# Kernel tuning notes

Measured on AMD Instinct MI355X. Metric: run time of the kernel, lower is better.

The kernel has to match this reference:

```python
import jax, jax.numpy as jnp
import numpy as np

ALPHA = 1.5
TEMPERATURE = 1.0
N_ITER = 25
N_EMBED = 2048
NUM_EXPERTS = 64
N_TOKENS = 32768


def entmax_bisect(X, alpha=ALPHA, n_iter=N_ITER):
    """Faithful port of entmax.entmax_bisect forward (dim=-1)."""
    d = X.shape[-1]
    inv = 1.0 / (alpha - 1.0)
    Xa = X * (alpha - 1.0)
    max_val = jnp.max(Xa, axis=-1, keepdims=True)
    # _gp(1, alpha) = 1 ; _gp(1/d, alpha) = (1/d)**(1/(alpha-1))
    tau_lo = max_val - 1.0
    tau_hi = max_val - (1.0 / d) ** inv

    def p(tau):
        return jnp.clip(Xa - tau, 0.0, None) ** inv

    f_lo = jnp.sum(p(tau_lo), axis=-1, keepdims=True) - 1.0
    dm0 = tau_hi - tau_lo

    def body(carry, _):
        tau_lo, dm = carry
        dm = dm * 0.5
        tau_m = tau_lo + dm
        p_m = p(tau_m)
        f_m = jnp.sum(p_m, axis=-1, keepdims=True) - 1.0
        mask = (f_m * f_lo) >= 0
        tau_lo = jnp.where(mask, tau_m, tau_lo)
        return (tau_lo, dm), tau_m

    (tau_lo, dm), tau_ms = jax.lax.scan(body, (tau_lo, dm0), None, length=n_iter)
    tau_m_last = tau_ms[-1]  # [..., 1] tau used for the returned p_m in torch loop
    p_m = p(tau_m_last)
    # ensure_sum_one
    p_m = p_m / jnp.sum(p_m, axis=-1, keepdims=True)
    return p_m


def setup_inputs() -> dict:
    key = jax.random.key(0)
    kx, kw, kb = jax.random.split(key, 3)
    x = jax.random.normal(kx, (N_TOKENS, N_EMBED), dtype=jnp.float32)
    # nn.Linear default init: U(-1/sqrt(fan_in), 1/sqrt(fan_in))
    bound = 1.0 / np.sqrt(N_EMBED)
    W = jax.random.uniform(kw, (NUM_EXPERTS, N_EMBED), dtype=jnp.float32, minval=-bound, maxval=bound)
    b = jax.random.uniform(kb, (NUM_EXPERTS,), dtype=jnp.float32, minval=-bound, maxval=bound)
    return {"x": x, "W": W, "b": b}


def reference(x, W, b):
    logits = jnp.einsum("td,ed->te", x, W) + b  # [T, E]
    scaled_logits = logits / TEMPERATURE
    return entmax_bisect(scaled_logits)
```

## Files before the change

kernel.cpp:

```cpp
#include <hip/hip_runtime.h>
#include <hip/hip_bf16.h>
#include <stdint.h>

typedef _Float16 half8 __attribute__((ext_vector_type(8)));
typedef float    f32x4 __attribute__((ext_vector_type(4)));

#define N_EMBED   2048
#define N_EXP     64
#define KCHUNK    64
#define NKC       (N_EMBED / KCHUNK)
#define GCH       16
#define TILEB     8192
#define LGT_STRIDE 68
#define LGT_FLOATS (64 * LGT_STRIDE)

__global__ __launch_bounds__(256) void convert_w_kernel(
        const float* __restrict__ W, uint8_t* __restrict__ wsimg) {
    int tid = blockIdx.x * 256 + threadIdx.x;
    int e   = tid >> 8;
    int d0  = (tid & 255) * 8;
    int kc  = d0 >> 6;
    int dd0 = d0 & 63;
    const float* src = W + e * N_EMBED + d0;
    float4 f0 = *(const float4*)(src);
    float4 f1 = *(const float4*)(src + 4);
    float v[8] = {f0.x, f0.y, f0.z, f0.w, f1.x, f1.y, f1.z, f1.w};
    union { _Float16 h[8]; uint4 u; } hv;
#pragma unroll
    for (int j = 0; j < 8; ++j) hv.h[j] = (_Float16)(0.5f * v[j]);
    uint32_t off = (uint32_t)((e * 128 + dd0 * 2) ^ ((e & 7) << 4));
    *(uint4*)(wsimg + (size_t)kc * TILEB + off) = hv.u;
}

__device__ __forceinline__ half8 cvt8(const float4& p, const float4& q) {
    half8 h;
    h[0] = (_Float16)p.x; h[1] = (_Float16)p.y;
    h[2] = (_Float16)p.z; h[3] = (_Float16)p.w;
    h[4] = (_Float16)q.x; h[5] = (_Float16)q.y;
    h[6] = (_Float16)q.z; h[7] = (_Float16)q.w;
    return h;
}

__global__ __launch_bounds__(512, 4) void router_kernel(
        const float* __restrict__ x, const uint8_t* __restrict__ img,
        const float* __restrict__ bias, float* __restrict__ out) {
    __shared__ uint8_t lds[2 * LGT_FLOATS * 4];

    const int tid  = threadIdx.x;
    const int wave = tid >> 6;
    const int lane = tid & 63;
    const int l15  = lane & 15;
    const int l4   = lane >> 4;
    const int g    = wave >> 2;
    const int q    = wave & 3;
    const int rowbase = blockIdx.x * 64;
    const float* xrow = x + (size_t)(rowbase + q * 16 + l15) * N_EMBED
                          + g * (GCH * KCHUNK) + l4 * 8;
    uint8_t* lbase = lds + g * 2 * TILEB;

    uint32_t boff[4][2];
#pragma unroll
    for (int t = 0; t < 4; ++t)
#pragma unroll
        for (int s = 0; s < 2; ++s)
            boff[t][s] = (uint32_t)(((16 * t + l15) * 128 + s * 64 + l4 * 16)
                                    ^ ((l15 & 7) << 4));

    f32x4 acc[4];
#pragma unroll
    for (int t = 0; t < 4; ++t) acc[t] = (f32x4){0.f, 0.f, 0.f, 0.f};

    const int tg  = tid >> 8;
    const int t8  = tid & 255;
    auto STAGE = [&](int i, int buf) {
        const uint8_t* gsrc = img + (size_t)(tg * GCH + i) * TILEB;
        uint8_t* dst = lds + tg * 2 * TILEB + buf * TILEB;
#pragma unroll
        for (int j = 0; j < 2; ++j) {
            __builtin_amdgcn_global_load_lds(
                (const __attribute__((address_space(1))) void*)(gsrc + j * 4096 + t8 * 16),
                (__attribute__((address_space(3))) void*)(dst + j * 4096 + t8 * 16),
                16, 0, 0);
        }
    };
    auto LOADA = [&](int i, float4& a0, float4& a1, float4& a2, float4& a3) {
        const float* ap = xrow + i * KCHUNK;
        a0 = *(const float4*)(ap);
        a1 = *(const float4*)(ap + 4);
        a2 = *(const float4*)(ap + 32);
        a3 = *(const float4*)(ap + 36);
    };
    auto MFMAS = [&](int buf, const half8& a0, const half8& a1) {
        const uint8_t* lb = lbase + (size_t)buf * TILEB;
#pragma unroll
        for (int s = 0; s < 2; ++s) {
            half8 ah = s ? a1 : a0;
#pragma unroll
            for (int t = 0; t < 4; ++t) {
                half8 bh = *(const half8*)(lb + boff[t][s]);
                acc[t] = __builtin_amdgcn_mfma_f32_16x16x32_f16(ah, bh, acc[t], 0, 0, 0);
            }
        }
    };

    float4 A0, A1, A2, A3, B0, B1, B2, B3;

    STAGE(0, 0);
    __builtin_amdgcn_sched_barrier(0);
    LOADA(0, A0, A1, A2, A3);
    LOADA(1, B0, B1, B2, B3);
    __builtin_amdgcn_sched_barrier(0);
    asm volatile("s_waitcnt vmcnt(8)" ::: "memory");
    __builtin_amdgcn_s_barrier();
    __builtin_amdgcn_sched_barrier(0);

#pragma unroll 1
    for (int i = 0; i < GCH - 2; i += 2) {
        STAGE(i + 1, (i + 1) & 1);
        __builtin_amdgcn_sched_barrier(0);
        {
            half8 a0 = cvt8(A0, A1);
            half8 a1 = cvt8(A2, A3);
            LOADA(i + 2, A0, A1, A2, A3);
            MFMAS(i & 1, a0, a1);
        }
        asm volatile("s_waitcnt vmcnt(4) lgkmcnt(0)" ::: "memory");
        __builtin_amdgcn_s_barrier();
        __builtin_amdgcn_sched_barrier(0);

        STAGE(i + 2, i & 1);
        __builtin_amdgcn_sched_barrier(0);
        {
            half8 a0 = cvt8(B0, B1);
            half8 a1 = cvt8(B2, B3);
            LOADA(i + 3, B0, B1, B2, B3);
            MFMAS((i + 1) & 1, a0, a1);
        }
        asm volatile("s_waitcnt vmcnt(4) lgkmcnt(0)" ::: "memory");
        __builtin_amdgcn_s_barrier();
        __builtin_amdgcn_sched_barrier(0);
    }

    STAGE(GCH - 1, 1);
    __builtin_amdgcn_sched_barrier(0);
    {
        half8 a0 = cvt8(A0, A1);
        half8 a1 = cvt8(A2, A3);
        MFMAS(0, a0, a1);
    }
    asm volatile("s_waitcnt vmcnt(0) lgkmcnt(0)" ::: "memory");
    __builtin_amdgcn_s_barrier();
    __builtin_amdgcn_sched_barrier(0);
    {
        half8 a0 = cvt8(B0, B1);
        half8 a1 = cvt8(B2, B3);
        MFMAS(1, a0, a1);
    }

    __syncthreads();
    {
        float* lgt = (float*)lds + g * LGT_FLOATS;
#pragma unroll
        for (int t = 0; t < 4; ++t)
#pragma unroll
            for (int r = 0; r < 4; ++r)
                lgt[(q * 16 + l4 * 4 + r) * LGT_STRIDE + t * 16 + l15] = acc[t][r];
    }
    __syncthreads();

    const float* L0 = (const float*)lds;
    const float* L1 = L0 + LGT_FLOATS;
    const int row_local = wave * 8 + (lane >> 3);
    const int eb = (lane & 7) * 8;
    const int base = row_local * LGT_STRIDE + eb;

    float v[8];
    {
        float4 u0 = *(const float4*)(L0 + base);
        float4 u1 = *(const float4*)(L0 + base + 4);
        float4 w0 = *(const float4*)(L1 + base);
        float4 w1 = *(const float4*)(L1 + base + 4);
        float4 c0 = *(const float4*)(bias + eb);
        float4 c1 = *(const float4*)(bias + eb + 4);
        v[0] = u0.x + w0.x + 0.5f * c0.x;
        v[1] = u0.y + w0.y + 0.5f * c0.y;
        v[2] = u0.z + w0.z + 0.5f * c0.z;
        v[3] = u0.w + w0.w + 0.5f * c0.w;
        v[4] = u1.x + w1.x + 0.5f * c1.x;
        v[5] = u1.y + w1.y + 0.5f * c1.y;
        v[6] = u1.z + w1.z + 0.5f * c1.z;
        v[7] = u1.w + w1.w + 0.5f * c1.w;
    }

    float m = v[0];
#pragma unroll
    for (int j = 1; j < 8; ++j) m = fmaxf(m, v[j]);
    m = fmaxf(m, __shfl_xor(m, 1, 64));
    m = fmaxf(m, __shfl_xor(m, 2, 64));
    m = fmaxf(m, __shfl_xor(m, 4, 64));

    float tau_lo = m - 1.0f;
    float tau_hi = m - 0.000244140625f;
    float dm = tau_hi - tau_lo;

    float s0 = 0.f;
#pragma unroll
    for (int j = 0; j < 8; ++j) {
        float d = fmaxf(v[j] - tau_lo, 0.f);
        s0 = fmaf(d, d, s0);
    }
    s0 += __shfl_xor(s0, 1, 64);
    s0 += __shfl_xor(s0, 2, 64);
    s0 += __shfl_xor(s0, 4, 64);
    const float f_lo = s0 - 1.0f;

    float tau_m = tau_lo, fsum = 1.0f;
#pragma unroll 1
    for (int it = 0; it < 25; ++it) {
        dm *= 0.5f;
        tau_m = tau_lo + dm;
        float s = 0.f;
#pragma unroll
        for (int j = 0; j < 8; ++j) {
            float d = fmaxf(v[j] - tau_m, 0.f);
            s = fmaf(d, d, s);
        }
        s += __shfl_xor(s, 1, 64);
        s += __shfl_xor(s, 2, 64);
        s += __shfl_xor(s, 4, 64);
        if ((s - 1.0f) * f_lo >= 0.0f) tau_lo = tau_m;
        fsum = s;
    }
    float rinv = 1.0f / fsum;
    float4 o0, o1;
    {
        float d;
        d = fmaxf(v[0] - tau_m, 0.f); o0.x = d * d * rinv;
        d = fmaxf(v[1] - tau_m, 0.f); o0.y = d * d * rinv;
        d = fmaxf(v[2] - tau_m, 0.f); o0.z = d * d * rinv;
        d = fmaxf(v[3] - tau_m, 0.f); o0.w = d * d * rinv;
        d = fmaxf(v[4] - tau_m, 0.f); o1.x = d * d * rinv;
        d = fmaxf(v[5] - tau_m, 0.f); o1.y = d * d * rinv;
        d = fmaxf(v[6] - tau_m, 0.f); o1.z = d * d * rinv;
        d = fmaxf(v[7] - tau_m, 0.f); o1.w = d * d * rinv;
    }
    float* op = out + (size_t)(rowbase + row_local) * N_EXP + eb;
    *(float4*)(op)     = o0;
    *(float4*)(op + 4) = o1;
}

extern "C" void kernel_launch(void* const* d_in, const int* in_sizes, int n_in,
                              void* d_out, int out_size, void* d_ws, size_t ws_size,
                              hipStream_t stream) {
    (void)n_in; (void)out_size; (void)ws_size;
    const float* x  = (const float*)d_in[0];
    const float* W  = (const float*)d_in[1];
    const float* b  = (const float*)d_in[2];
    float* out      = (float*)d_out;
    uint8_t* wsimg  = (uint8_t*)d_ws;

    const int T = in_sizes[0] / N_EMBED;

    convert_w_kernel<<<dim3(64), dim3(256), 0, stream>>>(W, wsimg);
    router_kernel<<<dim3(T / 64), dim3(512), 0, stream>>>(x, wsimg, b, out);
}
```

Measured before the change: 63.20 us.

## Deepen weight-tile LDS pipeline from double to quad buffering

Replaces the two-slot LDS buffer for weight tiles with a four-slot ring per group, prefetching three tiles ahead and loosening the vmcnt waits so more global-to-LDS loads stay in flight during the MFMA loop. The epilogue is restructured to drain the deeper pipeline. The goal is to hide the latency of weight loads. In exchange LDS use per block grows to 64 KB, which may reduce how many blocks fit on a CU, and the hand-tuned waitcnt values must exactly match the outstanding load counts.

Measured after the change: 60.79 us. 1.04x faster.

```diff
diff --git a/kernel.cpp b/kernel.cpp
--- a/kernel.cpp
+++ b/kernel.cpp
@@ -44,7 +44,7 @@
 __global__ __launch_bounds__(512, 4) void router_kernel(
         const float* __restrict__ x, const uint8_t* __restrict__ img,
         const float* __restrict__ bias, float* __restrict__ out) {
-    __shared__ uint8_t lds[2 * LGT_FLOATS * 4];
+    __shared__ uint8_t lds[65536];
 
     const int tid  = threadIdx.x;
     const int wave = tid >> 6;
@@ -56,7 +56,7 @@
     const int rowbase = blockIdx.x * 64;
     const float* xrow = x + (size_t)(rowbase + q * 16 + l15) * N_EMBED
                           + g * (GCH * KCHUNK) + l4 * 8;
-    uint8_t* lbase = lds + g * 2 * TILEB;
+    uint8_t* gring = lds + g * (4 * TILEB);
 
     uint32_t boff[4][2];
 #pragma unroll
@@ -72,9 +72,9 @@
 
     const int tg  = tid >> 8;
     const int t8  = tid & 255;
-    auto STAGE = [&](int i, int buf) {
+    auto STAGE = [&](int i) {
         const uint8_t* gsrc = img + (size_t)(tg * GCH + i) * TILEB;
-        uint8_t* dst = lds + tg * 2 * TILEB + buf * TILEB;
+        uint8_t* dst = lds + tg * (4 * TILEB) + (i & 3) * TILEB;
 #pragma unroll
         for (int j = 0; j < 2; ++j) {
             __builtin_amdgcn_global_load_lds(
@@ -90,8 +90,8 @@
         a2 = *(const float4*)(ap + 32);
         a3 = *(const float4*)(ap + 36);
     };
-    auto MFMAS = [&](int buf, const half8& a0, const half8& a1) {
-        const uint8_t* lb = lbase + (size_t)buf * TILEB;
+    auto MFMAS = [&](int slot, const half8& a0, const half8& a1) {
+        const uint8_t* lb = gring + (size_t)slot * TILEB;
 #pragma unroll
         for (int s = 0; s < 2; ++s) {
             half8 ah = s ? a1 : a0;
@@ -105,56 +105,77 @@
 
     float4 A0, A1, A2, A3, B0, B1, B2, B3;
 
-    STAGE(0, 0);
+    STAGE(0); STAGE(1); STAGE(2);
     __builtin_amdgcn_sched_barrier(0);
     LOADA(0, A0, A1, A2, A3);
     LOADA(1, B0, B1, B2, B3);
     __builtin_amdgcn_sched_barrier(0);
-    asm volatile("s_waitcnt vmcnt(8)" ::: "memory");
+    asm volatile("s_waitcnt vmcnt(12)" ::: "memory");
     __builtin_amdgcn_s_barrier();
     __builtin_amdgcn_sched_barrier(0);
 
 #pragma unroll 1
-    for (int i = 0; i < GCH - 2; i += 2) {
-        STAGE(i + 1, (i + 1) & 1);
+    for (int i = 0; i < 12; i += 2) {
+        STAGE(i + 3);
         __builtin_amdgcn_sched_barrier(0);
         {
             half8 a0 = cvt8(A0, A1);
             half8 a1 = cvt8(A2, A3);
             LOADA(i + 2, A0, A1, A2, A3);
-            MFMAS(i & 1, a0, a1);
-        }
-        asm volatile("s_waitcnt vmcnt(4) lgkmcnt(0)" ::: "memory");
+            MFMAS(i & 3, a0, a1);
+        }
+        asm volatile("s_waitcnt vmcnt(16) lgkmcnt(0)" ::: "memory");
         __builtin_amdgcn_s_barrier();
         __builtin_amdgcn_sched_barrier(0);
 
-        STAGE(i + 2, i & 1);
+        STAGE(i + 4);
         __builtin_amdgcn_sched_barrier(0);
         {
             half8 a0 = cvt8(B0, B1);
             half8 a1 = cvt8(B2, B3);
             LOADA(i + 3, B0, B1, B2, B3);
-            MFMAS((i + 1) & 1, a0, a1);
-        }
-        asm volatile("s_waitcnt vmcnt(4) lgkmcnt(0)" ::: "memory");
+            MFMAS((i + 1) & 3, a0, a1);
+        }
+        asm volatile("s_waitcnt vmcnt(16) lgkmcnt(0)" ::: "memory");
         __builtin_amdgcn_s_barrier();
         __builtin_amdgcn_sched_barrier(0);
     }
 
-    STAGE(GCH - 1, 1);
+    STAGE(15);
     __builtin_amdgcn_sched_barrier(0);
     {
         half8 a0 = cvt8(A0, A1);
         half8 a1 = cvt8(A2, A3);
+        LOADA(14, A0, A1, A2, A3);
         MFMAS(0, a0, a1);
     }
-    asm volatile("s_waitcnt vmcnt(0) lgkmcnt(0)" ::: "memory");
-    __builtin_amdgcn_s_barrier();
-    __builtin_amdgcn_sched_barrier(0);
+    asm volatile("s_waitcnt vmcnt(16) lgkmcnt(0)" ::: "memory");
+    __builtin_amdgcn_s_barrier();
+    __builtin_amdgcn_sched_barrier(0);
+
     {
         half8 a0 = cvt8(B0, B1);
         half8 a1 = cvt8(B2, B3);
+        LOADA(15, B0, B1, B2, B3);
         MFMAS(1, a0, a1);
+    }
+    asm volatile("s_waitcnt vmcnt(14) lgkmcnt(0)" ::: "memory");
+    __builtin_amdgcn_s_barrier();
+    __builtin_amdgcn_sched_barrier(0);
+
+    {
+        half8 a0 = cvt8(A0, A1);
+        half8 a1 = cvt8(A2, A3);
+        MFMAS(2, a0, a1);
+    }
+    asm volatile("s_waitcnt vmcnt(8) lgkmcnt(0)" ::: "memory");
+    __builtin_amdgcn_s_barrier();
+    __builtin_amdgcn_sched_barrier(0);
+
+    {
+        half8 a0 = cvt8(B0, B1);
+        half8 a1 = cvt8(B2, B3);
+        MFMAS(3, a0, a1);
     }
 
     __syncthreads();
```

## Double K-chunk granularity per pipeline stage with 4-slot LDS ring

Applied to the files above, without the earlier changes.

Each pipeline step now stages two K-chunks of the weight image into a four-slot LDS ring per group and loads two chunks of x per register set. This halves the number of barrier/waitcnt steps per block and puts more loads in flight to hide global latency. In exchange, LDS grows to 64 KB per block and register use for the x prefetch doubles. Both could cut occupancy below the four blocks per CU that the launch bounds request.

Result: slower. 176.2 us (+178.8%).

```diff
diff --git a/kernel.cpp b/kernel.cpp
--- a/kernel.cpp
+++ b/kernel.cpp
@@ -10,6 +10,7 @@
 #define KCHUNK    64
 #define NKC       (N_EMBED / KCHUNK)
 #define GCH       16
+#define NPAIR     8
 #define TILEB     8192
 #define LGT_STRIDE 68
 #define LGT_FLOATS (64 * LGT_STRIDE)
@@ -44,7 +45,7 @@
 __global__ __launch_bounds__(512, 4) void router_kernel(
         const float* __restrict__ x, const uint8_t* __restrict__ img,
         const float* __restrict__ bias, float* __restrict__ out) {
-    __shared__ uint8_t lds[2 * LGT_FLOATS * 4];
+    __shared__ uint8_t lds[65536];
 
     const int tid  = threadIdx.x;
     const int wave = tid >> 6;
@@ -56,7 +57,7 @@
     const int rowbase = blockIdx.x * 64;
     const float* xrow = x + (size_t)(rowbase + q * 16 + l15) * N_EMBED
                           + g * (GCH * KCHUNK) + l4 * 8;
-    uint8_t* lbase = lds + g * 2 * TILEB;
+    uint8_t* gring = lds + g * (4 * TILEB);
 
     uint32_t boff[4][2];
 #pragma unroll
@@ -72,89 +73,105 @@
 
     const int tg  = tid >> 8;
     const int t8  = tid & 255;
-    auto STAGE = [&](int i, int buf) {
-        const uint8_t* gsrc = img + (size_t)(tg * GCH + i) * TILEB;
-        uint8_t* dst = lds + tg * 2 * TILEB + buf * TILEB;
-#pragma unroll
-        for (int j = 0; j < 2; ++j) {
-            __builtin_amdgcn_global_load_lds(
-                (const __attribute__((address_space(1))) void*)(gsrc + j * 4096 + t8 * 16),
-                (__attribute__((address_space(3))) void*)(dst + j * 4096 + t8 * 16),
-                16, 0, 0);
+    auto STAGE2 = [&](int p) {
+#pragma unroll
+        for (int c = 0; c < 2; ++c) {
+            int kc = 2 * p + c;
+            const uint8_t* gsrc = img + (size_t)(tg * GCH + kc) * TILEB;
+            uint8_t* dst = lds + tg * (4 * TILEB) + (kc & 3) * TILEB;
+#pragma unroll
+            for (int j = 0; j < 2; ++j) {
+                __builtin_amdgcn_global_load_lds(
+                    (const __attribute__((address_space(1))) void*)(gsrc + j * 4096 + t8 * 16),
+                    (__attribute__((address_space(3))) void*)(dst + j * 4096 + t8 * 16),
+                    16, 0, 0);
+            }
         }
     };
-    auto LOADA = [&](int i, float4& a0, float4& a1, float4& a2, float4& a3) {
-        const float* ap = xrow + i * KCHUNK;
-        a0 = *(const float4*)(ap);
-        a1 = *(const float4*)(ap + 4);
-        a2 = *(const float4*)(ap + 32);
-        a3 = *(const float4*)(ap + 36);
+    auto LOADA2 = [&](int p, float4 A[8]) {
+        const float* ap = xrow + 2 * p * KCHUNK;
+        A[0] = *(const float4*)(ap);
+        A[1] = *(const float4*)(ap + 4);
+        A[2] = *(const float4*)(ap + 32);
+        A[3] = *(const float4*)(ap + 36);
+        A[4] = *(const float4*)(ap + 64);
+        A[5] = *(const float4*)(ap + 68);
+        A[6] = *(const float4*)(ap + 96);
+        A[7] = *(const float4*)(ap + 100);
     };
-    auto MFMAS = [&](int buf, const half8& a0, const half8& a1) {
-        const uint8_t* lb = lbase + (size_t)buf * TILEB;
-#pragma unroll
-        for (int s = 0; s < 2; ++s) {
-            half8 ah = s ? a1 : a0;
-#pragma unroll
-            for (int t = 0; t < 4; ++t) {
-                half8 bh = *(const half8*)(lb + boff[t][s]);
-                acc[t] = __builtin_amdgcn_mfma_f32_16x16x32_f16(ah, bh, acc[t], 0, 0, 0);
+    auto MFMAS2 = [&](int p, const half8 a[4]) {
+#pragma unroll
+        for (int c = 0; c < 2; ++c) {
+            const uint8_t* lb = gring + (size_t)((2 * p + c) & 3) * TILEB;
+#pragma unroll
+            for (int s = 0; s < 2; ++s) {
+                half8 ah = a[2 * c + s];
+#pragma unroll
+                for (int t = 0; t < 4; ++t) {
+                    half8 bh = *(const half8*)(lb + boff[t][s]);
+                    acc[t] = __builtin_amdgcn_mfma_f32_16x16x32_f16(ah, bh, acc[t], 0, 0, 0);
+                }
             }
         }
     };
 
-    float4 A0, A1, A2, A3, B0, B1, B2, B3;
-
-    STAGE(0, 0);
-    __builtin_amdgcn_sched_barrier(0);
-    LOADA(0, A0, A1, A2, A3);
-    LOADA(1, B0, B1, B2, B3);
-    __builtin_amdgcn_sched_barrier(0);
-    asm volatile("s_waitcnt vmcnt(8)" ::: "memory");
+    float4 Aa[8], Ab[8];
+
+    STAGE2(0);
+    __builtin_amdgcn_sched_barrier(0);
+    LOADA2(0, Aa);
+    LOADA2(1, Ab);
+    __builtin_amdgcn_sched_barrier(0);
+    asm volatile("s_waitcnt vmcnt(16)" ::: "memory");
     __builtin_amdgcn_s_barrier();
     __builtin_amdgcn_sched_barrier(0);
 
 #pragma unroll 1
-    for (int i = 0; i < GCH - 2; i += 2) {
-        STAGE(i + 1, (i + 1) & 1);
+    for (int p = 0; p < 6; p += 2) {
+        STAGE2(p + 1);
         __builtin_amdgcn_sched_barrier(0);
         {
-            half8 a0 = cvt8(A0, A1);
-            half8 a1 = cvt8(A2, A3);
-            LOADA(i + 2, A0, A1, A2, A3);
-            MFMAS(i & 1, a0, a1);
-        }
-        asm volatile("s_waitcnt vmcnt(4) lgkmcnt(0)" ::: "memory");
+            half8 a[4];
+            a[0] = cvt8(Aa[0], Aa[1]); a[1] = cvt8(Aa[2], Aa[3]);
+            a[2] = cvt8(Aa[4], Aa[5]); a[3] = cvt8(Aa[6], Aa[7]);
+            LOADA2(p + 2, Aa);
+            MFMAS2(p, a);
+        }
+        asm volatile("s_waitcnt vmcnt(8) lgkmcnt(0)" ::: "memory");
         __builtin_amdgcn_s_barrier();
         __builtin_amdgcn_sched_barrier(0);
 
-        STAGE(i + 2, i & 1);
+        STAGE2(p + 2);
         __builtin_amdgcn_sched_barrier(0);
         {
-            half8 a0 = cvt8(B0, B1);
-            half8 a1 = cvt8(B2, B3);
-            LOADA(i + 3, B0, B1, B2, B3);
-            MFMAS((i + 1) & 1, a0, a1);
-        }
-        asm volatile("s_waitcnt vmcnt(4) lgkmcnt(0)" ::: "memory");
+            half8 a[4];
+            a[0] = cvt8(Ab[0], Ab[1]); a[1] = cvt8(Ab[2], Ab[3]);
+            a[2] = cvt8(Ab[4], Ab[5]); a[3] = cvt8(Ab[6], Ab[7]);
+            LOADA2(p + 3, Ab);
+            MFMAS2(p + 1, a);
+        }
+        asm volatile("s_waitcnt vmcnt(8) lgkmcnt(0)" ::: "memory");
         __builtin_amdgcn_s_barrier();
         __builtin_amdgcn_sched_barrier(0);
     }
 
-    STAGE(GCH - 1, 1);
-    __builtin_amdgcn_sched_barrier(0);
-    {
-        half8 a0 = cvt8(A0, A1);
-        half8 a1 = cvt8(A2, A3);
-        MFMAS(0, a0, a1);
+    STAGE2(7);
+    __builtin_amdgcn_sched_barrier(0);
+    {
+        half8 a[4];
+        a[0] = cvt8(Aa[0], Aa[1]); a[1] = cvt8(Aa[2], Aa[3]);
+        a[2] = cvt8(Aa[4], Aa[5]); a[3] = cvt8(Aa[6], Aa[7]);
+        MFMAS2(6, a);
     }
     asm volatile("s_waitcnt vmcnt(0) lgkmcnt(0)" ::: "memory");
     __builtin_amdgcn_s_barrier();
     __builtin_amdgcn_sched_barrier(0);
-    {
-        half8 a0 = cvt8(B0, B1);
-        half8 a1 = cvt8(B2, B3);
-        MFMAS(1, a0, a1);
+
+    {
+        half8 a[4];
+        a[0] = cvt8(Ab[0], Ab[1]); a[1] = cvt8(Ab[2], Ab[3]);
+        a[2] = cvt8(Ab[4], Ab[5]); a[3] = cvt8(Ab[6], Ab[7]);
+        MFMAS2(7, a);
     }
 
     __syncthreads();
```

## Stage two K-chunks per barrier using a four-slot LDS ring

Applied to the files above, without the earlier changes.

Replaces the two-buffer, one-chunk-per-step pipeline with a four-slot LDS ring per K-group. Each iteration stages two weight chunks and loads two chunks of x, so only half as many barriers and waitcnt stalls are needed. LDS per block grows to 64 KiB, which can reduce the number of resident blocks per CU and so weaken latency hiding in this bandwidth-bound GEMM. The entmax logit array is also unrolled into scalar registers, which changes little.

Measured after the change: 59.31 us. 6.2% less time.

```diff
diff --git a/kernel.cpp b/kernel.cpp
--- a/kernel.cpp
+++ b/kernel.cpp
@@ -44,7 +44,7 @@
 __global__ __launch_bounds__(512, 4) void router_kernel(
         const float* __restrict__ x, const uint8_t* __restrict__ img,
         const float* __restrict__ bias, float* __restrict__ out) {
-    __shared__ uint8_t lds[2 * LGT_FLOATS * 4];
+    __shared__ uint8_t lds[65536];
 
     const int tid  = threadIdx.x;
     const int wave = tid >> 6;
@@ -56,7 +56,7 @@
     const int rowbase = blockIdx.x * 64;
     const float* xrow = x + (size_t)(rowbase + q * 16 + l15) * N_EMBED
                           + g * (GCH * KCHUNK) + l4 * 8;
-    uint8_t* lbase = lds + g * 2 * TILEB;
+    uint8_t* gring = lds + g * (4 * TILEB);
 
     uint32_t boff[4][2];
 #pragma unroll
@@ -72,89 +72,90 @@
 
     const int tg  = tid >> 8;
     const int t8  = tid & 255;
-    auto STAGE = [&](int i, int buf) {
-        const uint8_t* gsrc = img + (size_t)(tg * GCH + i) * TILEB;
-        uint8_t* dst = lds + tg * 2 * TILEB + buf * TILEB;
-#pragma unroll
-        for (int j = 0; j < 2; ++j) {
-            __builtin_amdgcn_global_load_lds(
-                (const __attribute__((address_space(1))) void*)(gsrc + j * 4096 + t8 * 16),
-                (__attribute__((address_space(3))) void*)(dst + j * 4096 + t8 * 16),
-                16, 0, 0);
+    auto STAGE2 = [&](int p) {
+#pragma unroll
+        for (int c = 0; c < 2; ++c) {
+            int kc = 2 * p + c;
+            const uint8_t* gsrc = img + (size_t)(tg * GCH + kc) * TILEB;
+            uint8_t* dst = lds + tg * (4 * TILEB) + (kc & 3) * TILEB;
+#pragma unroll
+            for (int j = 0; j < 2; ++j) {
+                __builtin_amdgcn_global_load_lds(
+                    (const __attribute__((address_space(1))) void*)(gsrc + j * 4096 + t8 * 16),
+                    (__attribute__((address_space(3))) void*)(dst + j * 4096 + t8 * 16),
+                    16, 0, 0);
+            }
         }
     };
-    auto LOADA = [&](int i, float4& a0, float4& a1, float4& a2, float4& a3) {
-        const float* ap = xrow + i * KCHUNK;
-        a0 = *(const float4*)(ap);
-        a1 = *(const float4*)(ap + 4);
-        a2 = *(const float4*)(ap + 32);
-        a3 = *(const float4*)(ap + 36);
+
+    float4 A0, A1, A2, A3, A4, A5, A6, A7;
+    auto LOADA2 = [&](int p) {
+        const float* ap = xrow + 2 * p * KCHUNK;
+        A0 = *(const float4*)(ap);
+        A1 = *(const float4*)(ap + 4);
+        A2 = *(const float4*)(ap + 32);
+        A3 = *(const float4*)(ap + 36);
+        A4 = *(const float4*)(ap + 64);
+        A5 = *(const float4*)(ap + 68);
+        A6 = *(const float4*)(ap + 96);
+        A7 = *(const float4*)(ap + 100);
     };
-    auto MFMAS = [&](int buf, const half8& a0, const half8& a1) {
-        const uint8_t* lb = lbase + (size_t)buf * TILEB;
-#pragma unroll
-        for (int s = 0; s < 2; ++s) {
-            half8 ah = s ? a1 : a0;
-#pragma unroll
-            for (int t = 0; t < 4; ++t) {
-                half8 bh = *(const half8*)(lb + boff[t][s]);
-                acc[t] = __builtin_amdgcn_mfma_f32_16x16x32_f16(ah, bh, acc[t], 0, 0, 0);
-            }
+    auto MFMAS2 = [&](int p, half8 a0, half8 a1, half8 a2, half8 a3) {
+        const uint8_t* lb0 = gring + (size_t)((2 * p) & 3) * TILEB;
+        const uint8_t* lb1 = gring + (size_t)((2 * p + 1) & 3) * TILEB;
+#pragma unroll
+        for (int t = 0; t < 4; ++t) {
+            half8 bh = *(const half8*)(lb0 + boff[t][0]);
+            acc[t] = __builtin_amdgcn_mfma_f32_16x16x32_f16(a0, bh, acc[t], 0, 0, 0);
+        }
+#pragma unroll
+        for (int t = 0; t < 4; ++t) {
+            half8 bh = *(const half8*)(lb0 + boff[t][1]);
+            acc[t] = __builtin_amdgcn_mfma_f32_16x16x32_f16(a1, bh, acc[t], 0, 0, 0);
+        }
+#pragma unroll
+        for (int t = 0; t < 4; ++t) {
+            half8 bh = *(const half8*)(lb1 + boff[t][0]);
+            acc[t] = __builtin_amdgcn_mfma_f32_16x16x32_f16(a2, bh, acc[t], 0, 0, 0);
+        }
+#pragma unroll
+        for (int t = 0; t < 4; ++t) {
+            half8 bh = *(const half8*)(lb1 + boff[t][1]);
+            acc[t] = __builtin_amdgcn_mfma_f32_16x16x32_f16(a3, bh, acc[t], 0, 0, 0);
         }
     };
 
-    float4 A0, A1, A2, A3, B0, B1, B2, B3;
-
-    STAGE(0, 0);
+    STAGE2(0);
     __builtin_amdgcn_sched_barrier(0);
-    LOADA(0, A0, A1, A2, A3);
-    LOADA(1, B0, B1, B2, B3);
+    LOADA2(0);
     __builtin_amdgcn_sched_barrier(0);
     asm volatile("s_waitcnt vmcnt(8)" ::: "memory");
     __builtin_amdgcn_s_barrier();
     __builtin_amdgcn_sched_barrier(0);
 
 #pragma unroll 1
-    for (int i = 0; i < GCH - 2; i += 2) {
-        STAGE(i + 1, (i + 1) & 1);
+    for (int p = 0; p < 7; ++p) {
+        STAGE2(p + 1);
         __builtin_amdgcn_sched_barrier(0);
         {
             half8 a0 = cvt8(A0, A1);
             half8 a1 = cvt8(A2, A3);
-            LOADA(i + 2, A0, A1, A2, A3);
-            MFMAS(i & 1, a0, a1);
-        }
-        asm volatile("s_waitcnt vmcnt(4) lgkmcnt(0)" ::: "memory");
+            half8 a2 = cvt8(A4, A5);
+            half8 a3 = cvt8(A6, A7);
+            LOADA2(p + 1);
+            MFMAS2(p, a0, a1, a2, a3);
+        }
+        asm volatile("s_waitcnt vmcnt(8) lgkmcnt(0)" ::: "memory");
         __builtin_amdgcn_s_barrier();
         __builtin_amdgcn_sched_barrier(0);
-
-        STAGE(i + 2, i & 1);
-        __builtin_amdgcn_sched_barrier(0);
-        {
-            half8 a0 = cvt8(B0, B1);
-            half8 a1 = cvt8(B2, B3);
-            LOADA(i + 3, B0, B1, B2, B3);
-            MFMAS((i + 1) & 1, a0, a1);
-        }
-        asm volatile("s_waitcnt vmcnt(4) lgkmcnt(0)" ::: "memory");
-        __builtin_amdgcn_s_barrier();
-        __builtin_amdgcn_sched_barrier(0);
-    }
-
-    STAGE(GCH - 1, 1);
-    __builtin_amdgcn_sched_barrier(0);
+    }
+
     {
         half8 a0 = cvt8(A0, A1);
         half8 a1 = cvt8(A2, A3);
-        MFMAS(0, a0, a1);
-    }
-    asm volatile("s_waitcnt vmcnt(0) lgkmcnt(0)" ::: "memory");
-    __builtin_amdgcn_s_barrier();
-    __builtin_amdgcn_sched_barrier(0);
-    {
-        half8 a0 = cvt8(B0, B1);
-        half8 a1 = cvt8(B2, B3);
-        MFMAS(1, a0, a1);
+        half8 a2 = cvt8(A4, A5);
+        half8 a3 = cvt8(A6, A7);
+        MFMAS2(7, a0, a1, a2, a3);
     }
 
     __syncthreads();
@@ -174,7 +175,7 @@
     const int eb = (lane & 7) * 8;
     const int base = row_local * LGT_STRIDE + eb;
 
-    float v[8];
+    float v0, v1, v2, v3, v4, v5, v6, v7;
     {
         float4 u0 = *(const float4*)(L0 + base);
         float4 u1 = *(const float4*)(L0 + base + 4);
@@ -182,19 +183,18 @@
         float4 w1 = *(const float4*)(L1 + base + 4);
         float4 c0 = *(const float4*)(bias + eb);
         float4 c1 = *(const float4*)(bias + eb + 4);
-        v[0] = u0.x + w0.x + 0.5f * c0.x;
-        v[1] = u0.y + w0.y + 0.5f * c0.y;
-        v[2] = u0.z + w0.z + 0.5f * c0.z;
-        v[3] = u0.w + w0.w + 0.5f * c0.w;
-        v[4] = u1.x + w1.x + 0.5f * c1.x;
-        v[5] = u1.y + w1.y + 0.5f * c1.y;
-        v[6] = u1.z + w1.z + 0.5f * c1.z;
-        v[7] = u1.w + w1.w + 0.5f * c1.w;
-    }
-
-    float m = v[0];
-#pragma unroll
-    for (int j = 1; j < 8; ++j) m = fmaxf(m, v[j]);
+        v0 = u0.x + w0.x + 0.5f * c0.x;
+        v1 = u0.y + w0.y + 0.5f * c0.y;
+        v2 = u0.z + w0.z + 0.5f * c0.z;
+        v3 = u0.w + w0.w + 0.5f * c0.w;
+        v4 = u1.x + w1.x + 0.5f * c1.x;
+        v5 = u1.y + w1.y + 0.5f * c1.y;
+        v6 = u1.z + w1.z + 0.5f * c1.z;
+        v7 = u1.w + w1.w + 0.5f * c1.w;
+    }
+
+    float m = fmaxf(fmaxf(fmaxf(v0, v1), fmaxf(v2, v3)),
+                    fmaxf(fmaxf(v4, v5), fmaxf(v6, v7)));
     m = fmaxf(m, __shfl_xor(m, 1, 64));
     m = fmaxf(m, __shfl_xor(m, 2, 64));
     m = fmaxf(m, __shfl_xor(m, 4, 64));
@@ -203,11 +203,17 @@
     float tau_hi = m - 0.000244140625f;
     float dm = tau_hi - tau_lo;
 
-    float s0 = 0.f;
-#pragma unroll
-    for (int j = 0; j < 8; ++j) {
-        float d = fmaxf(v[j] - tau_lo, 0.f);
-        s0 = fmaf(d, d, s0);
+    float s0;
+    {
+        float d;
+        d = fmaxf(v0 - tau_lo, 0.f); s0 = d * d;
+        d = fmaxf(v1 - tau_lo, 0.f); s0 = fmaf(d, d, s0);
+        d = fmaxf(v2 - tau_lo, 0.f); s0 = fmaf(d, d, s0);
+        d = fmaxf(v3 - tau_lo, 0.f); s0 = fmaf(d, d, s0);
+        d = fmaxf(v4 - tau_lo, 0.f); s0 = fmaf(d, d, s0);
+        d = fmaxf(v5 - tau_lo, 0.f); s0 = fmaf(d, d, s0);
+        d = fmaxf(v6 - tau_lo, 0.f); s0 = fmaf(d, d, s0);
+        d = fmaxf(v7 - tau_lo, 0.f); s0 = fmaf(d, d, s0);
     }
     s0 += __shfl_xor(s0, 1, 64);
     s0 += __shfl_xor(s0, 2, 64);
@@ -219,12 +225,15 @@
     for (int it = 0; it < 25; ++it) {
         dm *= 0.5f;
         tau_m = tau_lo + dm;
-        float s = 0.f;
-#pragma unroll
-        for (int j = 0; j < 8; ++j) {
-            float d = fmaxf(v[j] - tau_m, 0.f);
-            s = fmaf(d, d, s);
-        }
+        float s, d;
+        d = fmaxf(v0 - tau_m, 0.f); s = d * d;
+        d = fmaxf(v1 - tau_m, 0.f); s = fmaf(d, d, s);
+        d = fmaxf(v2 - tau_m, 0.f); s = fmaf(d, d, s);
+        d = fmaxf(v3 - tau_m, 0.f); s = fmaf(d, d, s);
+        d = fmaxf(v4 - tau_m, 0.f); s = fmaf(d, d, s);
+        d = fmaxf(v5 - tau_m, 0.f); s = fmaf(d, d, s);
+        d = fmaxf(v6 - tau_m, 0.f); s = fmaf(d, d, s);
+        d = fmaxf(v7 - tau_m, 0.f); s = fmaf(d, d, s);
         s += __shfl_xor(s, 1, 64);
         s += __shfl_xor(s, 2, 64);
         s += __shfl_xor(s, 4, 64);
@@ -235,14 +244,14 @@
     float4 o0, o1;
     {
         float d;
-        d = fmaxf(v[0] - tau_m, 0.f); o0.x = d * d * rinv;
-        d = fmaxf(v[1] - tau_m, 0.f); o0.y = d * d * rinv;
-        d = fmaxf(v[2] - tau_m, 0.f); o0.z = d * d * rinv;
-        d = fmaxf(v[3] - tau_m, 0.f); o0.w = d * d * rinv;
-        d = fmaxf(v[4] - tau_m, 0.f); o1.x = d * d * rinv;
-        d = fmaxf(v[5] - tau_m, 0.f); o1.y = d * d * rinv;
-        d = fmaxf(v[6] - tau_m, 0.f); o1.z = d * d * rinv;
-        d = fmaxf(v[7] - tau_m, 0.f); o1.w = d * d * rinv;
+        d = fmaxf(v0 - tau_m, 0.f); o0.x = d * d * rinv;
+        d = fmaxf(v1 - tau_m, 0.f); o0.y = d * d * rinv;
+        d = fmaxf(v2 - tau_m, 0.f); o0.z = d * d * rinv;
+        d = fmaxf(v3 - tau_m, 0.f); o0.w = d * d * rinv;
+        d = fmaxf(v4 - tau_m, 0.f); o1.x = d * d * rinv;
+        d = fmaxf(v5 - tau_m, 0.f); o1.y = d * d * rinv;
+        d = fmaxf(v6 - tau_m, 0.f); o1.z = d * d * rinv;
+        d = fmaxf(v7 - tau_m, 0.f); o1.w = d * d * rinv;
     }
     float* op = out + (size_t)(rowbase + row_local) * N_EXP + eb;
     *(float4*)(op)     = o0;
```
